# Kernel optimization log

Measured on AMD Instinct MI355X. Metric: run time of the kernel, lower is better.

Reference implementation:

```python
import jax, jax.numpy as jnp
import numpy as np

S = 3      # num_scales
CIN = 3    # in_channels (hardcoded by expand(...,3,...) in source)
COUT = 3   # out_channels (forced by final broadcast)
K = 3
PAD = 1


def setup_inputs() -> dict:
    key = jax.random.key(0)
    ks = jax.random.split(key, 8)
    B, H, W = 4, 384, 384
    x = jax.random.normal(ks[0], (B, CIN, H, W), jnp.float32)
    # params follow the torch inits: theta,sigma ~ U(0,pi); f0,theta0 = 1
    theta = jax.random.uniform(ks[1], (S, COUT, CIN), jnp.float32) * jnp.pi
    sigma = jax.random.uniform(ks[2], (S, COUT, CIN), jnp.float32) * jnp.pi
    f0 = jnp.ones((S, COUT, CIN), jnp.float32)
    theta0 = jnp.ones((S, COUT, CIN), jnp.float32)
    attn_w1 = jax.random.normal(ks[3], (64, CIN), jnp.float32) * 0.1     # 1x1 conv weight
    attn_b1 = jnp.zeros((64,), jnp.float32)
    attn_w2 = jax.random.normal(ks[4], (COUT * S, 64), jnp.float32) * 0.1
    attn_b2 = jnp.zeros((COUT * S,), jnp.float32)
    conv_w = jax.random.normal(ks[5], (COUT, CIN, K, K), jnp.float32) * 0.05
    mixing = jax.random.uniform(ks[6], (1,), jnp.float32)
    band = jax.random.uniform(ks[7], (COUT, CIN, 2), jnp.float32)        # freq_band_select ~ U(0,1)
    return dict(x=x, theta=theta, sigma=sigma, f0=f0, theta0=theta0,
                attn_w1=attn_w1, attn_b1=attn_b1, attn_w2=attn_w2, attn_b2=attn_b2,
                conv_w=conv_w, mixing=mixing, band=band)


def _log_gabor_bank(theta, sigma, f0, theta0, H, W):
    # vectorized over all scales: returns [S, Co, Cin, H, W] real filter bank
    yy, xx = jnp.meshgrid(jnp.linspace(-1.0, 1.0, H), jnp.linspace(-1.0, 1.0, W), indexing='ij')
    r = jnp.sqrt(xx * xx + yy * yy + 1e-6)          # [H,W]
    phi = jnp.arctan2(yy, xx)                        # [H,W]
    f0e = f0[..., None, None]                        # [S,Co,Cin,1,1]
    sig = sigma[..., None, None]
    th = theta[..., None, None]
    th0 = theta0[..., None, None]
    log_gabor = jnp.exp(-jnp.log(r - jnp.log(f0e)) ** 2 / (2.0 * jnp.log(sig) ** 2))
    angular = jnp.exp(-(phi - th) ** 2 / (2.0 * th0 ** 2))
    return log_gabor * angular


def _forward(x, theta, sigma, f0, theta0, attn_w1, attn_b1, attn_w2, attn_b2, conv_w, mixing, band):
    B, Cin, H, W = x.shape
    # torch.fft.fftshift with no dim shifts ALL axes (incl. batch/channel) -- replicate exactly
    x_freq_shift = jnp.fft.fftshift(jnp.fft.fft2(x))                 # [B,Cin,H,W] complex64

    filt = _log_gabor_bank(theta, sigma, f0, theta0, H, W)           # [S,Co,Cin,H,W]

    # attention net: 1x1 conv -> relu -> 1x1 conv -> softmax over channel dim
    mag = jnp.abs(x_freq_shift)
    h1 = jax.nn.relu(jnp.einsum('bchw,oc->bohw', mag, attn_w1) + attn_b1[None, :, None, None])
    logits = jnp.einsum('bchw,oc->bohw', h1, attn_w2) + attn_b2[None, :, None, None]
    attn = jax.nn.softmax(logits, axis=1).reshape(B, S, COUT, H, W)

    # attended[b,d,h,w] = sum_{s,co} attn[b,s,co,h,w] * xfreq[b,d,h,w] * filt[s,co,d,h,w]
    wgt = jnp.einsum('bschw,scdhw->bdhw', attn, filt)                # real [B,Cin,H,W]
    attended = (x_freq_shift * wgt).sum(axis=1)                      # [B,H,W] complex

    # per-(out,in)-channel square band mask, indices from height (as in source)
    start_idx = jnp.floor((band[..., 0] + 1.0) / 2.0 * H).astype(jnp.int32)   # [Co,Cin]
    end_idx = jnp.floor((band[..., 1] + 1.0) / 2.0 * H).astype(jnp.int32)
    ih = jnp.arange(H)
    rm = (ih[None, None, :] >= start_idx[..., None]) & (ih[None, None, :] < end_idx[..., None])
    iw = jnp.arange(W)
    cm = (iw[None, None, :] >= start_idx[..., None]) & (iw[None, None, :] < end_idx[..., None])
    mask = (rm[..., :, None] & cm[..., None, :]).astype(x.dtype)     # [Co,Cin,H,W]

    # broadcast quirk in source: [B,1,H,W] * [B,Co,1,Cin,H,W] -> [B,Co,B,Cin,H,W]
    six = mask[None, :, None, :, :, :] * attended[None, None, :, None, :, :]
    six = jnp.broadcast_to(six, (B, COUT, B, Cin, H, W))
    # torch ifftshift with no dim shifts ALL 6 axes; ifft2 transforms last two
    x_filtered = jnp.fft.ifft2(jnp.fft.ifftshift(six)).real          # [B,Co,B,Cin,H,W]

    x_spatial = jax.lax.conv_general_dilated(
        x, conv_w, window_strides=(1, 1), padding=[(PAD, PAD), (PAD, PAD)],
        dimension_numbers=('NCHW', 'OIHW', 'NCHW'))                  # [B,Co,H,W]

    mix = mixing[0]
    return mix * x_filtered + (1.0 - mix) * x_spatial[None, None]    # [B,Co,B,Cin,H,W]


def reference(x, theta, sigma, f0, theta0, attn_w1, attn_b1, attn_w2, attn_b2, conv_w, mixing, band):
    return _forward(x, theta, sigma, f0, theta0, attn_w1, attn_b1, attn_w2, attn_b2, conv_w, mixing, band)
```

## Files before the change

kernel.cpp:

```cpp
#include <hip/hip_runtime.h>
#include <math.h>

#define N384 384
#define NPIX 147456
#define LSTRIDE 385
#define LINES 8

__device__ __forceinline__ float2 cmul(float2 a, float2 b) {
    return make_float2(a.x*b.x - a.y*b.y, a.x*b.y + a.y*b.x);
}

__device__ __forceinline__ void build_tw(float2* tw, int tid) {
    for (int k = tid; k < 384; k += 256) {
        float sn, cs;
        sincospif((float)k * (2.0f / 384.0f), &sn, &cs);
        tw[k] = make_float2(cs, sn);
    }
}

template <int SGNI>
__device__ void fft384x8(float2* b0, float2* b1, const float2* tw, int tid) {
    float2* src = b0;
    float2* dst = b1;
    const int line = tid >> 5;
    const int l32  = tid & 31;

    {
        const float s3 = (float)SGNI * 0.86602540378443864676f;
        float2* L = src + line * LSTRIDE;
        float2* D = dst + line * LSTRIDE;
#pragma unroll
        for (int q = 0; q < 4; ++q) {
            int j = l32 + 32 * q;
            float2 a0 = L[j], a1 = L[j + 128], a2 = L[j + 256];
            float t1x = a1.x + a2.x, t1y = a1.y + a2.y;
            float t2x = a1.x - a2.x, t2y = a1.y - a2.y;
            float2 bb0 = make_float2(a0.x + t1x, a0.y + t1y);
            float mx = a0.x - 0.5f * t1x, my = a0.y - 0.5f * t1y;
            float ux = -s3 * t2y, uy = s3 * t2x;
            float2 bb1 = make_float2(mx + ux, my + uy);
            float2 bb2 = make_float2(mx - ux, my - uy);
            float2 t  = tw[j];
            float2 t2 = tw[2 * j];
            float2 w  = make_float2(t.x,  (float)SGNI * t.y);
            float2 w2 = make_float2(t2.x, (float)SGNI * t2.y);
            D[3 * j]     = bb0;
            D[3 * j + 1] = cmul(bb1, w);
            D[3 * j + 2] = cmul(bb2, w2);
        }
    }
    __syncthreads();
    { float2* t = src; src = dst; dst = t; }

#pragma unroll
    for (int st = 0; st < 7; ++st) {
        const int s  = 3 << st;
        const int n2 = 64 >> st;
        float2* L = src + line * LSTRIDE;
        float2* D = dst + line * LSTRIDE;
#pragma unroll
        for (int q = 0; q < 6; ++q) {
            int i = l32 + 32 * q;
            int j = i / s;
            int k = i - j * s;
            float2 a = L[k + s * j];
            float2 b = L[k + s * j + s * n2];
            float2 t = tw[j * s];
            float2 w = make_float2(t.x, (float)SGNI * t.y);
            float2 sum = make_float2(a.x + b.x, a.y + b.y);
            float2 dif = make_float2(a.x - b.x, a.y - b.y);
            D[k + s * (2 * j)]     = sum;
            D[k + s * (2 * j) + s] = cmul(dif, w);
        }
        __syncthreads();
        { float2* t = src; src = dst; dst = t; }
    }
}

__global__ __launch_bounds__(256) void k_fwd_rows(const float* __restrict__ x,
                                                  float2* __restrict__ F1) {
    __shared__ float2 sbuf[2][LINES * LSTRIDE];
    __shared__ float2 tw[384];
    int img = blockIdx.y;
    int rg  = blockIdx.x;
    int tid = threadIdx.x;
    build_tw(tw, tid);
    const float4* xim = (const float4*)(x + (size_t)img * NPIX + (size_t)rg * 8 * 384);
    for (int idx4 = tid; idx4 < 768; idx4 += 256) {
        int line = idx4 / 96;
        int e    = (idx4 - line * 96) * 4;
        float4 v = xim[idx4];
        float2* L = sbuf[0] + line * LSTRIDE + e;
        L[0] = make_float2(v.x, 0.0f);
        L[1] = make_float2(v.y, 0.0f);
        L[2] = make_float2(v.z, 0.0f);
        L[3] = make_float2(v.w, 0.0f);
    }
    __syncthreads();
    fft384x8<-1>(sbuf[0], sbuf[1], tw, tid);
    float4* o = (float4*)(F1 + (size_t)img * NPIX + (size_t)rg * 8 * 384);
    for (int idx4 = tid; idx4 < 1536; idx4 += 256) {
        int line = idx4 / 192;
        int e2   = (idx4 - line * 192) * 2;
        float2 a = sbuf[0][line * LSTRIDE + e2];
        float2 b = sbuf[0][line * LSTRIDE + e2 + 1];
        o[idx4] = make_float4(a.x, a.y, b.x, b.y);
    }
}

__global__ __launch_bounds__(256) void k_fwd_cols(const float2* __restrict__ In,
                                                  float2* __restrict__ Out) {
    __shared__ float2 sbuf[2][LINES * LSTRIDE];
    __shared__ float2 tw[384];
    int img = blockIdx.y;
    int cg  = blockIdx.x;
    int tid = threadIdx.x;
    build_tw(tw, tid);
    const float2* inim = In + (size_t)img * NPIX + cg * 8;
    int c = tid & 7, hb = tid >> 3;
    for (int q = 0; q < 12; ++q) {
        int h = hb + 32 * q;
        sbuf[0][c * LSTRIDE + h] = inim[(size_t)h * 384 + c];
    }
    __syncthreads();
    fft384x8<-1>(sbuf[0], sbuf[1], tw, tid);
    float2* outim = Out + (size_t)img * NPIX + cg * 8;
    for (int q = 0; q < 12; ++q) {
        int h = hb + 32 * q;
        outim[(size_t)h * 384 + c] = sbuf[0][c * LSTRIDE + h];
    }
}

__global__ __launch_bounds__(256) void k_attn(const float2* __restrict__ F2,
                                              const float* __restrict__ theta,
                                              const float* __restrict__ sigma,
                                              const float* __restrict__ f0,
                                              const float* __restrict__ theta0,
                                              const float* __restrict__ aw1,
                                              const float* __restrict__ ab1,
                                              const float* __restrict__ aw2,
                                              const float* __restrict__ ab2,
                                              float2* __restrict__ A) {
    __shared__ float4 par[27];
    int tid = threadIdx.x;
    if (tid < 27) {
        float lf0 = logf(f0[tid]);
        float ls  = logf(sigma[tid]);
        float na  = -0.5f / (ls * ls);
        float th  = theta[tid];
        float t0  = theta0[tid];
        float nb  = -0.5f / (t0 * t0);
        par[tid] = make_float4(lf0, na, th, nb);
    }
    __syncthreads();

    int p = blockIdx.x * 256 + tid;
    int h = p / 384;
    int w = p - h * 384;
    int hs = h + 192; if (hs >= 384) hs -= 384;
    int ws = w + 192; if (ws >= 384) ws -= 384;

    float2 xf[4][3];
    float  mag[4][3];
#pragma unroll
    for (int b = 0; b < 4; ++b) {
        int bp = (b + 2) & 3;
#pragma unroll
        for (int c = 0; c < 3; ++c) {
            int cp = c + 2; if (cp >= 3) cp -= 3;
            float2 v = F2[(size_t)(bp * 3 + cp) * NPIX + (size_t)hs * 384 + ws];
            xf[b][c]  = v;
            mag[b][c] = sqrtf(v.x * v.x + v.y * v.y);
        }
    }

    float lgt[4][9];
#pragma unroll
    for (int b = 0; b < 4; ++b)
#pragma unroll
        for (int j = 0; j < 9; ++j) lgt[b][j] = ab2[j];
    for (int o = 0; o < 64; ++o) {
        float w0 = aw1[o * 3 + 0], w1 = aw1[o * 3 + 1], w2 = aw1[o * 3 + 2];
        float bb = ab1[o];
        float hv[4];
#pragma unroll
        for (int b = 0; b < 4; ++b)
            hv[b] = fmaxf(bb + w0 * mag[b][0] + w1 * mag[b][1] + w2 * mag[b][2], 0.0f);
#pragma unroll
        for (int j = 0; j < 9; ++j) {
            float wj = aw2[j * 64 + o];
#pragma unroll
            for (int b = 0; b < 4; ++b) lgt[b][j] += wj * hv[b];
        }
    }

    float yy = -1.0f + 2.0f * (float)h / 383.0f;
    float xx = -1.0f + 2.0f * (float)w / 383.0f;
    float r   = sqrtf(xx * xx + yy * yy + 1e-6f);
    float phi = atan2f(yy, xx);
    float filt[27];
#pragma unroll
    for (int i = 0; i < 27; ++i) {
        float4 pr = par[i];
        float lr = logf(r - pr.x);
        float dphi = phi - pr.z;
        filt[i] = expf(lr * lr * pr.y + dphi * dphi * pr.w);
    }

#pragma unroll
    for (int b = 0; b < 4; ++b) {
        float mxv = lgt[b][0];
#pragma unroll
        for (int j = 1; j < 9; ++j) mxv = fmaxf(mxv, lgt[b][j]);
        float e[9];
        float se = 0.0f;
#pragma unroll
        for (int j = 0; j < 9; ++j) { e[j] = expf(lgt[b][j] - mxv); se += e[j]; }
        float inv = 1.0f / se;

        float2 acc = make_float2(0.0f, 0.0f);
#pragma unroll
        for (int d = 0; d < 3; ++d) {
            float wg = 0.0f;
#pragma unroll
            for (int s = 0; s < 3; ++s)
#pragma unroll
                for (int co = 0; co < 3; ++co)
                    wg += e[s * 3 + co] * filt[(s * 3 + co) * 3 + d];
            wg *= inv;
            acc.x += xf[b][d].x * wg;
            acc.y += xf[b][d].y * wg;
        }
        A[(size_t)b * NPIX + p] = acc;
    }
}

__global__ __launch_bounds__(256) void k_conv(const float* __restrict__ x,
                                              const float* __restrict__ cw,
                                              float* __restrict__ xsp) {
    int p = blockIdx.x * 256 + threadIdx.x;
    int w = p % 384;
    int t = p / 384;
    int h = t % 384; t /= 384;
    int o = t % 3;
    int b = t / 3;
    float acc = 0.0f;
    const float* xb = x + (size_t)b * 3 * NPIX;
#pragma unroll
    for (int ci = 0; ci < 3; ++ci) {
        const float* xc = xb + (size_t)ci * NPIX;
#pragma unroll
        for (int kh = 0; kh < 3; ++kh) {
            int hh = h + kh - 1;
            if (hh < 0 || hh >= 384) continue;
#pragma unroll
            for (int kw = 0; kw < 3; ++kw) {
                int ww = w + kw - 1;
                if (ww < 0 || ww >= 384) continue;
                acc += xc[(size_t)hh * 384 + ww] * cw[((o * 3 + ci) * 3 + kh) * 3 + kw];
            }
        }
    }
    xsp[p] = acc;
}

__global__ __launch_bounds__(256) void k_masked_rows(const float2* __restrict__ A,
                                                     const float* __restrict__ band,
                                                     float2* __restrict__ G1c) {
    int ii  = blockIdx.y;
    int rg  = blockIdx.x;
    int cop = ii / 12;
    int bp  = (ii / 3) % 4;
    int dp  = ii % 3;
    int pidx = (cop * 3 + dp) * 2;
    int sidx = (int)floorf((band[pidx + 0] + 1.0f) * 0.5f * 384.0f);
    int eidx = (int)floorf((band[pidx + 1] + 1.0f) * 0.5f * 384.0f);
    if (eidx <= sidx) return;
    int h0 = 192 + rg * 8;
    if (h0 + 8 <= sidx || h0 >= eidx) return;

    __shared__ float2 sbuf[2][LINES * LSTRIDE];
    __shared__ float2 tw[384];
    int tid = threadIdx.x;
    build_tw(tw, tid);
    const float2* Ab = A + (size_t)bp * NPIX;
    for (int idx = tid; idx < 8 * 384; idx += 256) {
        int line = idx / 384;
        int w    = idx - line * 384;
        int h    = h0 + line;
        bool m = (h >= sidx) && (h < eidx) && (w >= sidx) && (w < eidx);
        float2 v = make_float2(0.0f, 0.0f);
        if (m) v = Ab[(size_t)h * 384 + w];
        sbuf[0][line * LSTRIDE + w] = v;
    }
    __syncthreads();
    fft384x8<1>(sbuf[0], sbuf[1], tw, tid);
    for (int idx = tid; idx < 8 * 384; idx += 256) {
        int line = idx / 384;
        int w    = idx - line * 384;
        int h    = h0 + line;
        if (h >= sidx && h < eidx) {
            float2 v = sbuf[0][line * LSTRIDE + w];
            if (w & 1) { v.x = -v.x; v.y = -v.y; }
            G1c[((size_t)ii * 192 + (h - sidx)) * 384 + w] = v;
        }
    }
}

__global__ __launch_bounds__(256) void k_col_gemm_combine(const float2* __restrict__ G1c,
                                                          const float* __restrict__ band,
                                                          const float* __restrict__ xsp,
                                                          const float* __restrict__ mixing,
                                                          float* __restrict__ out) {
    int ii  = blockIdx.y;
    int gt  = blockIdx.x * 256 + threadIdx.x;
    int wq  = gt % 96;
    int hg  = gt / 96;
    int w   = wq * 4;
    int h0  = hg * 4;

    int cop = ii / 12;
    int bp  = (ii / 3) % 4;
    int dp  = ii % 3;
    int pidx = (cop * 3 + dp) * 2;
    int sidx = (int)floorf((band[pidx + 0] + 1.0f) * 0.5f * 384.0f);
    int eidx = (int)floorf((band[pidx + 1] + 1.0f) * 0.5f * 384.0f);

    float acc[4][4];
#pragma unroll
    for (int kh = 0; kh < 4; ++kh)
#pragma unroll
        for (int j = 0; j < 4; ++j) acc[kh][j] = 0.0f;

    const float4* g = (const float4*)(G1c + (size_t)ii * 192 * 384 + w);
    for (int hp = sidx; hp < eidx; ++hp) {
        float4 g0 = g[(size_t)(hp - sidx) * 192];
        float4 g1 = g[(size_t)(hp - sidx) * 192 + 1];
        int k0 = (hp * h0) % 384;
        float sn, cs;
        sincospif((float)k0 * (2.0f / 384.0f), &sn, &cs);
        float tx = cs, ty = sn;
        float ssn, scs;
        sincospif((float)hp * (2.0f / 384.0f), &ssn, &scs);
#pragma unroll
        for (int kh = 0; kh < 4; ++kh) {
            acc[kh][0] += tx * g0.x - ty * g0.y;
            acc[kh][1] += tx * g0.z - ty * g0.w;
            acc[kh][2] += tx * g1.x - ty * g1.y;
            acc[kh][3] += tx * g1.z - ty * g1.w;
            float ntx = tx * scs - ty * ssn;
            ty = tx * ssn + ty * scs;
            tx = ntx;
        }
    }

    int co = cop + 2; if (co >= 3) co -= 3;
    int b  = (bp + 2) & 3;
    int d  = dp + 2;  if (d >= 3) d -= 3;
    float mix  = mixing[0];
    float omix = 1.0f - mix;
    const float invn2 = 1.0f / 147456.0f;
    const float* xs = xsp + (size_t)(b * 3 + d) * NPIX;
    float* obase = out + (size_t)(co * 12 + b * 3 + d) * NPIX;
#pragma unroll
    for (int kh = 0; kh < 4; ++kh) {
        int h = h0 + kh;
        float sgn = (h & 1) ? -invn2 : invn2;
        size_t off = (size_t)h * 384 + w;
        float4 xv = *(const float4*)(xs + off);
        float4 val;
        val.x = mix * (acc[kh][0] * sgn) + omix * xv.x;
        val.y = mix * (acc[kh][1] * sgn) + omix * xv.y;
        val.z = mix * (acc[kh][2] * sgn) + omix * xv.z;
        val.w = mix * (acc[kh][3] * sgn) + omix * xv.w;
#pragma unroll
        for (int a = 0; a < 4; ++a)
            *(float4*)(obase + off + (size_t)a * 5308416) = val;
    }
}

extern "C" void kernel_launch(void* const* d_in, const int* in_sizes, int n_in,
                              void* d_out, int out_size, void* d_ws, size_t ws_size,
                              hipStream_t stream) {
    const float* x      = (const float*)d_in[0];
    const float* theta  = (const float*)d_in[1];
    const float* sigma  = (const float*)d_in[2];
    const float* f0     = (const float*)d_in[3];
    const float* theta0 = (const float*)d_in[4];
    const float* aw1    = (const float*)d_in[5];
    const float* ab1    = (const float*)d_in[6];
    const float* aw2    = (const float*)d_in[7];
    const float* ab2    = (const float*)d_in[8];
    const float* cw     = (const float*)d_in[9];
    const float* mixing = (const float*)d_in[10];
    const float* band   = (const float*)d_in[11];
    float* out = (float*)d_out;

    float2* F1  = (float2*)d_ws;
    float2* F2  = F1 + (size_t)12 * NPIX;
    float2* G1c = (float2*)d_ws;
    float2* A   = (float2*)d_ws + (size_t)36 * NPIX;
    float*  xsp = (float*)((float2*)d_ws + (size_t)40 * NPIX);

    k_fwd_rows<<<dim3(48, 12), 256, 0, stream>>>(x, F1);
    k_fwd_cols<<<dim3(48, 12), 256, 0, stream>>>(F1, F2);
    k_attn<<<576, 256, 0, stream>>>(F2, theta, sigma, f0, theta0,
                                    aw1, ab1, aw2, ab2, A);
    k_conv<<<6912, 256, 0, stream>>>(x, cw, xsp);
    k_masked_rows<<<dim3(24, 36), 256, 0, stream>>>(A, band, G1c);
    k_col_gemm_combine<<<dim3(36, 36), 256, 0, stream>>>(G1c, band, xsp, mixing, out);
}
```

Before: 238.7 us.

## Use radix-4 FFT stages, pack real rows pairwise, and table twiddles in column DFT

```diff
diff --git a/kernel.cpp b/kernel.cpp
--- a/kernel.cpp
+++ b/kernel.cpp
@@ -19,14 +19,15 @@
 }
 
 template <int SGNI>
-__device__ void fft384x8(float2* b0, float2* b1, const float2* tw, int tid) {
+__device__ float2* fft384x8(float2* b0, float2* b1, const float2* tw, int tid) {
     float2* src = b0;
     float2* dst = b1;
     const int line = tid >> 5;
     const int l32  = tid & 31;
+    const float SG = (float)SGNI;
 
     {
-        const float s3 = (float)SGNI * 0.86602540378443864676f;
+        const float s3 = SG * 0.86602540378443864676f;
         float2* L = src + line * LSTRIDE;
         float2* D = dst + line * LSTRIDE;
 #pragma unroll
@@ -42,8 +43,8 @@
             float2 bb2 = make_float2(mx - ux, my - uy);
             float2 t  = tw[j];
             float2 t2 = tw[2 * j];
-            float2 w  = make_float2(t.x,  (float)SGNI * t.y);
-            float2 w2 = make_float2(t2.x, (float)SGNI * t2.y);
+            float2 w  = make_float2(t.x,  SG * t.y);
+            float2 w2 = make_float2(t2.x, SG * t2.y);
             D[3 * j]     = bb0;
             D[3 * j + 1] = cmul(bb1, w);
             D[3 * j + 2] = cmul(bb2, w2);
@@ -53,28 +54,55 @@
     { float2* t = src; src = dst; dst = t; }
 
 #pragma unroll
-    for (int st = 0; st < 7; ++st) {
-        const int s  = 3 << st;
-        const int n2 = 64 >> st;
+    for (int st = 0; st < 3; ++st) {
+        const int s = 3 << (2 * st);
         float2* L = src + line * LSTRIDE;
         float2* D = dst + line * LSTRIDE;
 #pragma unroll
+        for (int q = 0; q < 3; ++q) {
+            int i = l32 + 32 * q;
+            int k = i % s;
+            int js = i - k;
+            float2 A0 = L[i];
+            float2 A1 = L[i + 96];
+            float2 A2 = L[i + 192];
+            float2 A3 = L[i + 288];
+            float t0x = A0.x + A2.x, t0y = A0.y + A2.y;
+            float t1x = A0.x - A2.x, t1y = A0.y - A2.y;
+            float t2x = A1.x + A3.x, t2y = A1.y + A3.y;
+            float t3x = A1.x - A3.x, t3y = A1.y - A3.y;
+            float u3x = -SG * t3y,   u3y = SG * t3x;
+            float2 y0 = make_float2(t0x + t2x, t0y + t2y);
+            float2 y2 = make_float2(t0x - t2x, t0y - t2y);
+            float2 y1 = make_float2(t1x + u3x, t1y + u3y);
+            float2 y3 = make_float2(t1x - u3x, t1y - u3y);
+            float2 c1 = tw[js], c2 = tw[2 * js], c3 = tw[3 * js];
+            float2 w1 = make_float2(c1.x, SG * c1.y);
+            float2 w2 = make_float2(c2.x, SG * c2.y);
+            float2 w3 = make_float2(c3.x, SG * c3.y);
+            int o = i + 3 * js;
+            D[o]         = y0;
+            D[o + s]     = cmul(y1, w1);
+            D[o + 2 * s] = cmul(y2, w2);
+            D[o + 3 * s] = cmul(y3, w3);
+        }
+        __syncthreads();
+        { float2* t = src; src = dst; dst = t; }
+    }
+
+    {
+        float2* L = src + line * LSTRIDE;
+        float2* D = dst + line * LSTRIDE;
+#pragma unroll
         for (int q = 0; q < 6; ++q) {
             int i = l32 + 32 * q;
-            int j = i / s;
-            int k = i - j * s;
-            float2 a = L[k + s * j];
-            float2 b = L[k + s * j + s * n2];
-            float2 t = tw[j * s];
-            float2 w = make_float2(t.x, (float)SGNI * t.y);
-            float2 sum = make_float2(a.x + b.x, a.y + b.y);
-            float2 dif = make_float2(a.x - b.x, a.y - b.y);
-            D[k + s * (2 * j)]     = sum;
-            D[k + s * (2 * j) + s] = cmul(dif, w);
-        }
-        __syncthreads();
-        { float2* t = src; src = dst; dst = t; }
-    }
+            float2 a = L[i], b = L[i + 192];
+            D[i]       = make_float2(a.x + b.x, a.y + b.y);
+            D[i + 192] = make_float2(a.x - b.x, a.y - b.y);
+        }
+    }
+    __syncthreads();
+    return dst;
 }
 
 __global__ __launch_bounds__(256) void k_fwd_rows(const float* __restrict__ x,
@@ -85,26 +113,28 @@
     int rg  = blockIdx.x;
     int tid = threadIdx.x;
     build_tw(tw, tid);
-    const float4* xim = (const float4*)(x + (size_t)img * NPIX + (size_t)rg * 8 * 384);
-    for (int idx4 = tid; idx4 < 768; idx4 += 256) {
-        int line = idx4 / 96;
-        int e    = (idx4 - line * 96) * 4;
+    const float4* xim = (const float4*)(x + (size_t)img * NPIX + (size_t)rg * 16 * 384);
+    for (int idx4 = tid; idx4 < 1536; idx4 += 256) {
+        int row = idx4 / 96;
+        int e   = (idx4 - row * 96) * 4;
         float4 v = xim[idx4];
-        float2* L = sbuf[0] + line * LSTRIDE + e;
-        L[0] = make_float2(v.x, 0.0f);
-        L[1] = make_float2(v.y, 0.0f);
-        L[2] = make_float2(v.z, 0.0f);
-        L[3] = make_float2(v.w, 0.0f);
-    }
-    __syncthreads();
-    fft384x8<-1>(sbuf[0], sbuf[1], tw, tid);
-    float4* o = (float4*)(F1 + (size_t)img * NPIX + (size_t)rg * 8 * 384);
-    for (int idx4 = tid; idx4 < 1536; idx4 += 256) {
-        int line = idx4 / 192;
-        int e2   = (idx4 - line * 192) * 2;
-        float2 a = sbuf[0][line * LSTRIDE + e2];
-        float2 b = sbuf[0][line * LSTRIDE + e2 + 1];
-        o[idx4] = make_float4(a.x, a.y, b.x, b.y);
+        float* L = (float*)(sbuf[0] + (row >> 1) * LSTRIDE + e) + (row & 1);
+        L[0] = v.x; L[2] = v.y; L[4] = v.z; L[6] = v.w;
+    }
+    __syncthreads();
+    float2* res = fft384x8<-1>(sbuf[0], sbuf[1], tw, tid);
+    float2* F1b = F1 + (size_t)img * NPIX + (size_t)rg * 16 * 384;
+    for (int it = tid; it < 3072; it += 256) {
+        int line = it / 384;
+        int k2   = it - line * 384;
+        const float2* L = res + line * LSTRIDE;
+        float2 A = L[k2];
+        int m = (k2 == 0) ? 0 : 384 - k2;
+        float2 B = L[m];
+        float2 X1 = make_float2(0.5f * (A.x + B.x), 0.5f * (A.y - B.y));
+        float2 X2 = make_float2(0.5f * (A.y + B.y), 0.5f * (B.x - A.x));
+        F1b[(size_t)(2 * line) * 384 + k2]     = X1;
+        F1b[(size_t)(2 * line + 1) * 384 + k2] = X2;
     }
 }
 
@@ -116,18 +146,22 @@
     int cg  = blockIdx.x;
     int tid = threadIdx.x;
     build_tw(tw, tid);
-    const float2* inim = In + (size_t)img * NPIX + cg * 8;
-    int c = tid & 7, hb = tid >> 3;
-    for (int q = 0; q < 12; ++q) {
-        int h = hb + 32 * q;
-        sbuf[0][c * LSTRIDE + h] = inim[(size_t)h * 384 + c];
-    }
-    __syncthreads();
-    fft384x8<-1>(sbuf[0], sbuf[1], tw, tid);
-    float2* outim = Out + (size_t)img * NPIX + cg * 8;
-    for (int q = 0; q < 12; ++q) {
-        int h = hb + 32 * q;
-        outim[(size_t)h * 384 + c] = sbuf[0][c * LSTRIDE + h];
+    const float4* inim = (const float4*)(In + (size_t)img * NPIX + cg * 8);
+    int c = tid & 3, hb = tid >> 2;
+    for (int q = 0; q < 6; ++q) {
+        int h = hb + 64 * q;
+        float4 v = inim[(size_t)h * 192 + c];
+        sbuf[0][(2 * c) * LSTRIDE + h]     = make_float2(v.x, v.y);
+        sbuf[0][(2 * c + 1) * LSTRIDE + h] = make_float2(v.z, v.w);
+    }
+    __syncthreads();
+    float2* res = fft384x8<-1>(sbuf[0], sbuf[1], tw, tid);
+    float4* outim = (float4*)(Out + (size_t)img * NPIX + cg * 8);
+    for (int q = 0; q < 6; ++q) {
+        int h = hb + 64 * q;
+        float2 a = res[(2 * c) * LSTRIDE + h];
+        float2 b = res[(2 * c + 1) * LSTRIDE + h];
+        outim[(size_t)h * 192 + c] = make_float4(a.x, a.y, b.x, b.y);
     }
 }
 
@@ -294,13 +328,13 @@
         sbuf[0][line * LSTRIDE + w] = v;
     }
     __syncthreads();
-    fft384x8<1>(sbuf[0], sbuf[1], tw, tid);
+    float2* res = fft384x8<1>(sbuf[0], sbuf[1], tw, tid);
     for (int idx = tid; idx < 8 * 384; idx += 256) {
         int line = idx / 384;
         int w    = idx - line * 384;
         int h    = h0 + line;
         if (h >= sidx && h < eidx) {
-            float2 v = sbuf[0][line * LSTRIDE + w];
+            float2 v = res[line * LSTRIDE + w];
             if (w & 1) { v.x = -v.x; v.y = -v.y; }
             G1c[((size_t)ii * 192 + (h - sidx)) * 384 + w] = v;
         }
@@ -312,8 +346,12 @@
                                                           const float* __restrict__ xsp,
                                                           const float* __restrict__ mixing,
                                                           float* __restrict__ out) {
+    __shared__ float2 tw[384];
+    int tid = threadIdx.x;
+    build_tw(tw, tid);
+
     int ii  = blockIdx.y;
-    int gt  = blockIdx.x * 256 + threadIdx.x;
+    int gt  = blockIdx.x * 256 + tid;
     int wq  = gt % 96;
     int hg  = gt / 96;
     int w   = wq * 4;
@@ -325,33 +363,48 @@
     int pidx = (cop * 3 + dp) * 2;
     int sidx = (int)floorf((band[pidx + 0] + 1.0f) * 0.5f * 384.0f);
     int eidx = (int)floorf((band[pidx + 1] + 1.0f) * 0.5f * 384.0f);
+    __syncthreads();
 
     float acc[4][4];
 #pragma unroll
     for (int kh = 0; kh < 4; ++kh)
 #pragma unroll
         for (int j = 0; j < 4; ++j) acc[kh][j] = 0.0f;
+
+    int idx0 = (sidx * (h0 + 0)) % 384;
+    int idx1 = (sidx * (h0 + 1)) % 384;
+    int idx2 = (sidx * (h0 + 2)) % 384;
+    int idx3 = (sidx * (h0 + 3)) % 384;
+    const int s0 = h0, s1 = h0 + 1, s2 = h0 + 2, s3 = h0 + 3;
 
     const float4* g = (const float4*)(G1c + (size_t)ii * 192 * 384 + w);
     for (int hp = sidx; hp < eidx; ++hp) {
         float4 g0 = g[(size_t)(hp - sidx) * 192];
         float4 g1 = g[(size_t)(hp - sidx) * 192 + 1];
-        int k0 = (hp * h0) % 384;
-        float sn, cs;
-        sincospif((float)k0 * (2.0f / 384.0f), &sn, &cs);
-        float tx = cs, ty = sn;
-        float ssn, scs;
-        sincospif((float)hp * (2.0f / 384.0f), &ssn, &scs);
-#pragma unroll
-        for (int kh = 0; kh < 4; ++kh) {
-            acc[kh][0] += tx * g0.x - ty * g0.y;
-            acc[kh][1] += tx * g0.z - ty * g0.w;
-            acc[kh][2] += tx * g1.x - ty * g1.y;
-            acc[kh][3] += tx * g1.z - ty * g1.w;
-            float ntx = tx * scs - ty * ssn;
-            ty = tx * ssn + ty * scs;
-            tx = ntx;
-        }
+        float2 t0 = tw[idx0];
+        float2 t1 = tw[idx1];
+        float2 t2 = tw[idx2];
+        float2 t3 = tw[idx3];
+        acc[0][0] += t0.x * g0.x - t0.y * g0.y;
+        acc[0][1] += t0.x * g0.z - t0.y * g0.w;
+        acc[0][2] += t0.x * g1.x - t0.y * g1.y;
+        acc[0][3] += t0.x * g1.z - t0.y * g1.w;
+        acc[1][0] += t1.x * g0.x - t1.y * g0.y;
+        acc[1][1] += t1.x * g0.z - t1.y * g0.w;
+        acc[1][2] += t1.x * g1.x - t1.y * g1.y;
+        acc[1][3] += t1.x * g1.z - t1.y * g1.w;
+        acc[2][0] += t2.x * g0.x - t2.y * g0.y;
+        acc[2][1] += t2.x * g0.z - t2.y * g0.w;
+        acc[2][2] += t2.x * g1.x - t2.y * g1.y;
+        acc[2][3] += t2.x * g1.z - t2.y * g1.w;
+        acc[3][0] += t3.x * g0.x - t3.y * g0.y;
+        acc[3][1] += t3.x * g0.z - t3.y * g0.w;
+        acc[3][2] += t3.x * g1.x - t3.y * g1.y;
+        acc[3][3] += t3.x * g1.z - t3.y * g1.w;
+        idx0 += s0; if (idx0 >= 384) idx0 -= 384;
+        idx1 += s1; if (idx1 >= 384) idx1 -= 384;
+        idx2 += s2; if (idx2 >= 384) idx2 -= 384;
+        idx3 += s3; if (idx3 >= 384) idx3 -= 384;
     }
 
     int co = cop + 2; if (co >= 3) co -= 3;
@@ -402,7 +455,7 @@
     float2* A   = (float2*)d_ws + (size_t)36 * NPIX;
     float*  xsp = (float*)((float2*)d_ws + (size_t)40 * NPIX);
 
-    k_fwd_rows<<<dim3(48, 12), 256, 0, stream>>>(x, F1);
+    k_fwd_rows<<<dim3(24, 12), 256, 0, stream>>>(x, F1);
     k_fwd_cols<<<dim3(48, 12), 256, 0, stream>>>(F1, F2);
     k_attn<<<576, 256, 0, stream>>>(F2, theta, sigma, f0, theta0,
                                     aw1, ab1, aw2, ab2, A);
```

Result: faster. 222.7 us (-6.7%).
